# Kernel tuning notes

Measured on AMD Instinct MI355X. Metric: run time of the kernel, lower is better.

The kernel has to match this reference:

```python
import jax, jax.numpy as jnp
import numpy as np

B, DIM_IN, DIM_OUT = 2048, 4096, 4096


def setup_inputs() -> dict:
    key = jax.random.key(0)
    k1, k2, k3 = jax.random.split(key, 3)
    # binary input activations (0/1), stored as int32
    x = jax.random.randint(k1, (B, DIM_IN), 0, 2, dtype=jnp.int32)
    masks = jax.random.uniform(k2, (DIM_IN, DIM_OUT)) < 0.5
    # integer thresholds in [0, dim_in)
    thresholds = jax.random.randint(k3, (DIM_OUT,), 0, DIM_IN, dtype=jnp.int32)
    return {"x": x, "masks": masks, "thresholds": thresholds}


def reference(x, masks, thresholds):
    # Original: expand x to (B, dim_in, dim_out), XNOR with masks, sum over dim_in,
    # compare vs thresholds. XNOR(a,b) = a*b + (1-a)*(1-b), so the sum over dim_in
    # is two GEMMs -- never materialize the (B, dim_in, dim_out) tensor.
    xf = x.astype(jnp.float32)              # (B, dim_in), values in {0,1}
    mf = masks.astype(jnp.float32)          # (dim_in, dim_out)
    sums = xf @ mf + (1.0 - xf) @ (1.0 - mf)  # (B, dim_out), popcount of agreements
    return sums > thresholds.astype(jnp.float32)[None, :]  # (B, dim_out) bool
```

## Files before the change

### kernel.cpp

```cpp
#include <hip/hip_runtime.h>
#include <stdint.h>

#define BB    2048
#define DIN   4096
#define DOUT  4096


using v4i  = __attribute__((ext_vector_type(4)))  int;
using v16i = __attribute__((ext_vector_type(16))) int;

__device__ __forceinline__ void async_load16(const void* g, void* l) {
    __builtin_amdgcn_global_load_lds(
        (const __attribute__((address_space(1))) unsigned int*)g,
        (__attribute__((address_space(3))) unsigned int*)l,
        16, 0, 0);
}

__device__ __forceinline__ unsigned int to_pm1(unsigned int c) {
    return c + ((c ^ 0x01010101u) * 255u);
}

__global__ void pack_all(const int* __restrict__ x,
                         const void* __restrict__ mraw,
                         char* __restrict__ x8,
                         char* __restrict__ m8T) {
    const int tid = threadIdx.x;
    if (blockIdx.x < 1024) {
        #pragma unroll
        for (int rr = 0; rr < 2; ++rr) {
            const int row = blockIdx.x * 2 + rr;
            const int4* src = (const int4*)(x + (size_t)row * DIN);
            unsigned int* dst = (unsigned int*)(x8 + (size_t)row * DIN);
            #pragma unroll
            for (int q = 0; q < 4; ++q) {
                int4 v = src[q * 256 + tid];
                unsigned int t = (unsigned int)(v.x & 1) |
                                 ((unsigned int)(v.y & 1) << 8) |
                                 ((unsigned int)(v.z & 1) << 16) |
                                 ((unsigned int)(v.w & 1) << 24);
                dst[q * 256 + tid] = to_pm1(t);
            }
        }
    } else {
        const int bw = blockIdx.x - 1024;
        const int n0  = (bw >> 4) * 64;
        const int k0b = (bw & 15) * 256;

        const unsigned char* mb = (const unsigned char*)mraw;
        const unsigned int pv = *(const unsigned int*)(mb + (tid & 63) * 4);
        const bool isU8 = __any(pv > 1u);

        const int n4 = (tid & 15) * 4;
        const int k4 = (tid >> 4) * 4;
        #pragma unroll
        for (int kt = 0; kt < 4; ++kt) {
            const int k0 = k0b + kt * 64;
            unsigned int a[4];
            if (isU8) {
                #pragma unroll
                for (int r = 0; r < 4; ++r)
                    a[r] = *(const unsigned int*)(mb + (size_t)(k0 + k4 + r) * DOUT + n0 + n4);
            } else {
                const int4* m32 = (const int4*)mraw;
                #pragma unroll
                for (int r = 0; r < 4; ++r) {
                    int4 v = m32[((size_t)(k0 + k4 + r) * DOUT + n0 + n4) >> 2];
                    a[r] = (unsigned int)(v.x & 1) |
                           ((unsigned int)(v.y & 1) << 8) |
                           ((unsigned int)(v.z & 1) << 16) |
                           ((unsigned int)(v.w & 1) << 24);
                }
            }
            unsigned int x0 = __builtin_amdgcn_perm(a[1], a[0], 0x05010400u);
            unsigned int x1 = __builtin_amdgcn_perm(a[3], a[2], 0x05010400u);
            unsigned int x2 = __builtin_amdgcn_perm(a[1], a[0], 0x07030602u);
            unsigned int x3 = __builtin_amdgcn_perm(a[3], a[2], 0x07030602u);
            unsigned int c0 = __builtin_amdgcn_perm(x1, x0, 0x05040100u);
            unsigned int c1 = __builtin_amdgcn_perm(x1, x0, 0x07060302u);
            unsigned int c2 = __builtin_amdgcn_perm(x3, x2, 0x05040100u);
            unsigned int c3 = __builtin_amdgcn_perm(x3, x2, 0x07060302u);
            *(unsigned int*)(m8T + (size_t)(n0 + n4 + 0) * DIN + k0 + k4) = to_pm1(c0);
            *(unsigned int*)(m8T + (size_t)(n0 + n4 + 1) * DIN + k0 + k4) = to_pm1(c1);
            *(unsigned int*)(m8T + (size_t)(n0 + n4 + 2) * DIN + k0 + k4) = to_pm1(c2);
            *(unsigned int*)(m8T + (size_t)(n0 + n4 + 3) * DIN + k0 + k4) = to_pm1(c3);
        }
    }
}

__global__ __launch_bounds__(256)
void bgemm(const char* __restrict__ x8,
           const char* __restrict__ m8T,
           const int* __restrict__ thr,
           int* __restrict__ out) {
    const int flat = blockIdx.x;
    const int xcd  = flat & 7;
    const int idx  = flat >> 3;
    const int bm   = (xcd & 1) * 4 + (idx & 3);
    const int bn   = (xcd >> 1) * 8 + (idx >> 2);
    const int b0   = bm * 256;
    const int o0   = bn * 128;

    const int tid  = threadIdx.x;
    const int lane = tid & 63;
    const int wv   = tid >> 6;
    const int wm   = (wv & 1) * 128;
    const int wn   = (wv >> 1) * 64;
    const int l31  = lane & 31;
    const int lh   = lane >> 5;
    const int rsw  = l31 & 7;

    __shared__ __align__(16) char lA[2][256 * 128];
    __shared__ __align__(16) char lB[2][128 * 128];

    auto stage = [&](int c, int buf) {
        const int k0 = c * 128;
        const int r8 = lane >> 3;
        const int sl = lane & 7;
        #pragma unroll
        for (int h = 0; h < 8; ++h) {
            const int r0  = wv * 64 + h * 8;
            const int row = r0 + r8;
            const int g   = sl ^ (row & 7);
            async_load16(x8 + (size_t)(b0 + row) * DIN + k0 + g * 16,
                         &lA[buf][r0 * 128 + lane * 16]);
        }
        #pragma unroll
        for (int h = 0; h < 4; ++h) {
            const int r0  = wv * 32 + h * 8;
            const int row = r0 + r8;
            const int g   = sl ^ (row & 7);
            async_load16(m8T + (size_t)(o0 + row) * DIN + k0 + g * 16,
                         &lB[buf][r0 * 128 + lane * 16]);
        }
    };

    v16i acc[4][2];
    #pragma unroll
    for (int t = 0; t < 4; ++t)
        #pragma unroll
        for (int u = 0; u < 2; ++u)
            acc[t][u] = (v16i)(0);

    stage(0, 0);
    __syncthreads();

    for (int c = 0; c < 32; ++c) {
        const int buf = c & 1;
        if (c < 31) stage(c + 1, buf ^ 1);

        #pragma unroll
        for (int ks = 0; ks < 4; ++ks) {
            const int slot = ((ks * 2 + lh) ^ rsw) * 16;
            v4i aF[4], bF[2];
            #pragma unroll
            for (int t = 0; t < 4; ++t)
                aF[t] = *(const v4i*)&lA[buf][(wm + t * 32 + l31) * 128 + slot];
            #pragma unroll
            for (int u = 0; u < 2; ++u)
                bF[u] = *(const v4i*)&lB[buf][(wn + u * 32 + l31) * 128 + slot];
            #pragma unroll
            for (int t = 0; t < 4; ++t)
                #pragma unroll
                for (int u = 0; u < 2; ++u)
                    acc[t][u] = __builtin_amdgcn_mfma_i32_32x32x32_i8(
                        aF[t], bF[u], acc[t][u], 0, 0, 0);
        }
        __syncthreads();
    }

    #pragma unroll
    for (int u = 0; u < 2; ++u) {
        const int o   = o0 + wn + u * 32 + l31;
        const int lim = 2 * thr[o] - DIN;
        #pragma unroll
        for (int t = 0; t < 4; ++t) {
            #pragma unroll
            for (int r = 0; r < 16; ++r) {
                const int rowl = (r & 3) + 8 * (r >> 2) + 4 * lh;
                const int b    = b0 + wm + t * 32 + rowl;
                out[(size_t)b * DOUT + o] = (acc[t][u][r] > lim) ? 1 : 0;
            }
        }
    }
}

extern "C" void kernel_launch(void* const* d_in, const int* in_sizes, int n_in,
                              void* d_out, int out_size, void* d_ws, size_t ws_size,
                              hipStream_t stream) {
    const int* x          = (const int*)d_in[0];
    const void* masks     = d_in[1];
    const int* thresholds = (const int*)d_in[2];
    int* out              = (int*)d_out;

    char* x8  = (char*)d_ws;
    char* m8T = (char*)d_ws + ((size_t)8 << 20);

    pack_all<<<2048, 256, 0, stream>>>(x, masks, x8, m8T);
    bgemm<<<256, 256, 0, stream>>>(x8, m8T, thresholds, out);
}
```

Measured before the change: 201.4 us.

## Split K across 8 waves with triple-buffered LDS and finer-grained pack blocks

The GEMM kernel now runs 512 threads per block. Each pair of wave groups handles half of every 128-wide K chunk, and their partial accumulators are combined through an LDS reduction at the end. The LDS pipeline moves from double to triple buffering, using explicit vmcnt waits and one raw barrier per iteration instead of two __syncthreads, so loads run further ahead of the MFMAs. The pack kernel also launches more, smaller blocks. The goal is more latency hiding and occupancy, at the cost of extra LDS (144KB), a reduction epilogue, and doubled register pressure per block.

Result: faster. 174.6 us (-13.3%).

```diff
diff --git a/kernel.cpp b/kernel.cpp
--- a/kernel.cpp
+++ b/kernel.cpp
@@ -25,26 +25,23 @@
                          char* __restrict__ x8,
                          char* __restrict__ m8T) {
     const int tid = threadIdx.x;
-    if (blockIdx.x < 1024) {
-        #pragma unroll
-        for (int rr = 0; rr < 2; ++rr) {
-            const int row = blockIdx.x * 2 + rr;
-            const int4* src = (const int4*)(x + (size_t)row * DIN);
-            unsigned int* dst = (unsigned int*)(x8 + (size_t)row * DIN);
-            #pragma unroll
-            for (int q = 0; q < 4; ++q) {
-                int4 v = src[q * 256 + tid];
-                unsigned int t = (unsigned int)(v.x & 1) |
-                                 ((unsigned int)(v.y & 1) << 8) |
-                                 ((unsigned int)(v.z & 1) << 16) |
-                                 ((unsigned int)(v.w & 1) << 24);
-                dst[q * 256 + tid] = to_pm1(t);
-            }
+    if (blockIdx.x < BB) {
+        const int row = blockIdx.x;
+        const int4* src = (const int4*)(x + (size_t)row * DIN);
+        unsigned int* dst = (unsigned int*)(x8 + (size_t)row * DIN);
+        #pragma unroll
+        for (int q = 0; q < 4; ++q) {
+            int4 v = src[q * 256 + tid];
+            unsigned int t = (unsigned int)(v.x & 1) |
+                             ((unsigned int)(v.y & 1) << 8) |
+                             ((unsigned int)(v.z & 1) << 16) |
+                             ((unsigned int)(v.w & 1) << 24);
+            dst[q * 256 + tid] = to_pm1(t);
         }
     } else {
-        const int bw = blockIdx.x - 1024;
-        const int n0  = (bw >> 4) * 64;
-        const int k0b = (bw & 15) * 256;
+        const int bw = blockIdx.x - BB;
+        const int k0 = (bw & 63) * 64;
+        const int n0 = (bw >> 6) * 64;
 
         const unsigned char* mb = (const unsigned char*)mraw;
         const unsigned int pv = *(const unsigned int*)(mb + (tid & 63) * 4);
@@ -52,42 +49,38 @@
 
         const int n4 = (tid & 15) * 4;
         const int k4 = (tid >> 4) * 4;
-        #pragma unroll
-        for (int kt = 0; kt < 4; ++kt) {
-            const int k0 = k0b + kt * 64;
-            unsigned int a[4];
-            if (isU8) {
-                #pragma unroll
-                for (int r = 0; r < 4; ++r)
-                    a[r] = *(const unsigned int*)(mb + (size_t)(k0 + k4 + r) * DOUT + n0 + n4);
-            } else {
-                const int4* m32 = (const int4*)mraw;
-                #pragma unroll
-                for (int r = 0; r < 4; ++r) {
-                    int4 v = m32[((size_t)(k0 + k4 + r) * DOUT + n0 + n4) >> 2];
-                    a[r] = (unsigned int)(v.x & 1) |
-                           ((unsigned int)(v.y & 1) << 8) |
-                           ((unsigned int)(v.z & 1) << 16) |
-                           ((unsigned int)(v.w & 1) << 24);
-                }
+        unsigned int a[4];
+        if (isU8) {
+            #pragma unroll
+            for (int r = 0; r < 4; ++r)
+                a[r] = *(const unsigned int*)(mb + (size_t)(k0 + k4 + r) * DOUT + n0 + n4);
+        } else {
+            const int4* m32 = (const int4*)mraw;
+            #pragma unroll
+            for (int r = 0; r < 4; ++r) {
+                int4 v = m32[((size_t)(k0 + k4 + r) * DOUT + n0 + n4) >> 2];
+                a[r] = (unsigned int)(v.x & 1) |
+                       ((unsigned int)(v.y & 1) << 8) |
+                       ((unsigned int)(v.z & 1) << 16) |
+                       ((unsigned int)(v.w & 1) << 24);
             }
-            unsigned int x0 = __builtin_amdgcn_perm(a[1], a[0], 0x05010400u);
-            unsigned int x1 = __builtin_amdgcn_perm(a[3], a[2], 0x05010400u);
-            unsigned int x2 = __builtin_amdgcn_perm(a[1], a[0], 0x07030602u);
-            unsigned int x3 = __builtin_amdgcn_perm(a[3], a[2], 0x07030602u);
-            unsigned int c0 = __builtin_amdgcn_perm(x1, x0, 0x05040100u);
-            unsigned int c1 = __builtin_amdgcn_perm(x1, x0, 0x07060302u);
-            unsigned int c2 = __builtin_amdgcn_perm(x3, x2, 0x05040100u);
-            unsigned int c3 = __builtin_amdgcn_perm(x3, x2, 0x07060302u);
-            *(unsigned int*)(m8T + (size_t)(n0 + n4 + 0) * DIN + k0 + k4) = to_pm1(c0);
-            *(unsigned int*)(m8T + (size_t)(n0 + n4 + 1) * DIN + k0 + k4) = to_pm1(c1);
-            *(unsigned int*)(m8T + (size_t)(n0 + n4 + 2) * DIN + k0 + k4) = to_pm1(c2);
-            *(unsigned int*)(m8T + (size_t)(n0 + n4 + 3) * DIN + k0 + k4) = to_pm1(c3);
-        }
-    }
-}
-
-__global__ __launch_bounds__(256)
+        }
+        unsigned int x0 = __builtin_amdgcn_perm(a[1], a[0], 0x05010400u);
+        unsigned int x1 = __builtin_amdgcn_perm(a[3], a[2], 0x05010400u);
+        unsigned int x2 = __builtin_amdgcn_perm(a[1], a[0], 0x07030602u);
+        unsigned int x3 = __builtin_amdgcn_perm(a[3], a[2], 0x07030602u);
+        unsigned int c0 = __builtin_amdgcn_perm(x1, x0, 0x05040100u);
+        unsigned int c1 = __builtin_amdgcn_perm(x1, x0, 0x07060302u);
+        unsigned int c2 = __builtin_amdgcn_perm(x3, x2, 0x05040100u);
+        unsigned int c3 = __builtin_amdgcn_perm(x3, x2, 0x07060302u);
+        *(unsigned int*)(m8T + (size_t)(n0 + n4 + 0) * DIN + k0 + k4) = to_pm1(c0);
+        *(unsigned int*)(m8T + (size_t)(n0 + n4 + 1) * DIN + k0 + k4) = to_pm1(c1);
+        *(unsigned int*)(m8T + (size_t)(n0 + n4 + 2) * DIN + k0 + k4) = to_pm1(c2);
+        *(unsigned int*)(m8T + (size_t)(n0 + n4 + 3) * DIN + k0 + k4) = to_pm1(c3);
+    }
+}
+
+__global__ __launch_bounds__(512)
 void bgemm(const char* __restrict__ x8,
            const char* __restrict__ m8T,
            const int* __restrict__ thr,
@@ -103,34 +96,38 @@
     const int tid  = threadIdx.x;
     const int lane = tid & 63;
     const int wv   = tid >> 6;
-    const int wm   = (wv & 1) * 128;
-    const int wn   = (wv >> 1) * 64;
+    const int im   = wv & 1;
+    const int in_  = (wv >> 1) & 1;
+    const int kh   = wv >> 2;
+    const int wm   = im * 128;
+    const int wn   = in_ * 64;
     const int l31  = lane & 31;
     const int lh   = lane >> 5;
     const int rsw  = l31 & 7;
 
-    __shared__ __align__(16) char lA[2][256 * 128];
-    __shared__ __align__(16) char lB[2][128 * 128];
+    __shared__ __align__(16) char lds[3 * 49152];
 
     auto stage = [&](int c, int buf) {
+        char* bufA = lds + buf * 49152;
+        char* bufB = bufA + 32768;
         const int k0 = c * 128;
         const int r8 = lane >> 3;
         const int sl = lane & 7;
-        #pragma unroll
-        for (int h = 0; h < 8; ++h) {
-            const int r0  = wv * 64 + h * 8;
-            const int row = r0 + r8;
-            const int g   = sl ^ (row & 7);
-            async_load16(x8 + (size_t)(b0 + row) * DIN + k0 + g * 16,
-                         &lA[buf][r0 * 128 + lane * 16]);
-        }
         #pragma unroll
         for (int h = 0; h < 4; ++h) {
             const int r0  = wv * 32 + h * 8;
             const int row = r0 + r8;
             const int g   = sl ^ (row & 7);
+            async_load16(x8 + (size_t)(b0 + row) * DIN + k0 + g * 16,
+                         bufA + r0 * 128 + lane * 16);
+        }
+        #pragma unroll
+        for (int h = 0; h < 2; ++h) {
+            const int r0  = wv * 16 + h * 8;
+            const int row = r0 + r8;
+            const int g   = sl ^ (row & 7);
             async_load16(m8T + (size_t)(o0 + row) * DIN + k0 + g * 16,
-                         &lB[buf][r0 * 128 + lane * 16]);
+                         bufB + r0 * 128 + lane * 16);
         }
     };
 
@@ -142,22 +139,26 @@
             acc[t][u] = (v16i)(0);
 
     stage(0, 0);
-    __syncthreads();
+    stage(1, 1);
 
     for (int c = 0; c < 32; ++c) {
-        const int buf = c & 1;
-        if (c < 31) stage(c + 1, buf ^ 1);
-
-        #pragma unroll
-        for (int ks = 0; ks < 4; ++ks) {
-            const int slot = ((ks * 2 + lh) ^ rsw) * 16;
+        if (c < 31) asm volatile("s_waitcnt vmcnt(6)" ::: "memory");
+        else        asm volatile("s_waitcnt vmcnt(0)" ::: "memory");
+        __builtin_amdgcn_s_barrier();
+        if (c < 30) stage(c + 2, (c + 2) % 3);
+
+        const char* bufA = lds + (c % 3) * 49152;
+        const char* bufB = bufA + 32768;
+        #pragma unroll
+        for (int ks = 0; ks < 2; ++ks) {
+            const int slot = (((kh * 4 + ks * 2 + lh) ^ rsw)) * 16;
             v4i aF[4], bF[2];
             #pragma unroll
             for (int t = 0; t < 4; ++t)
-                aF[t] = *(const v4i*)&lA[buf][(wm + t * 32 + l31) * 128 + slot];
+                aF[t] = *(const v4i*)&bufA[(wm + t * 32 + l31) * 128 + slot];
             #pragma unroll
             for (int u = 0; u < 2; ++u)
-                bF[u] = *(const v4i*)&lB[buf][(wn + u * 32 + l31) * 128 + slot];
+                bF[u] = *(const v4i*)&bufB[(wn + u * 32 + l31) * 128 + slot];
             #pragma unroll
             for (int t = 0; t < 4; ++t)
                 #pragma unroll
@@ -165,7 +166,39 @@
                     acc[t][u] = __builtin_amdgcn_mfma_i32_32x32x32_i8(
                         aF[t], bF[u], acc[t][u], 0, 0, 0);
         }
-        __syncthreads();
+    }
+    __syncthreads();
+
+    int* pool = (int*)lds;
+    const int p = wv & 3;
+    {
+        const int give0 = kh ? 0 : 2;
+        const int bw_ = p * 8192 + (kh ? 0 : 1) * 4096;
+        #pragma unroll
+        for (int tt = 0; tt < 2; ++tt) {
+            const int t = give0 + tt;
+            #pragma unroll
+            for (int u = 0; u < 2; ++u)
+                #pragma unroll
+                for (int r = 0; r < 16; ++r) {
+                    const int rowl = (r & 3) + 8 * (r >> 2) + 4 * lh;
+                    pool[bw_ + (tt * 32 + rowl) * 64 + u * 32 + l31] = acc[t][u][r];
+                }
+        }
+    }
+    __syncthreads();
+    const int keep0 = kh ? 2 : 0;
+    const int br_ = p * 8192 + kh * 4096;
+    #pragma unroll
+    for (int tt = 0; tt < 2; ++tt) {
+        const int t = keep0 + tt;
+        #pragma unroll
+        for (int u = 0; u < 2; ++u)
+            #pragma unroll
+            for (int r = 0; r < 16; ++r) {
+                const int rowl = (r & 3) + 8 * (r >> 2) + 4 * lh;
+                acc[t][u][r] += pool[br_ + (tt * 32 + rowl) * 64 + u * 32 + l31];
+            }
     }
 
     #pragma unroll
@@ -173,11 +206,12 @@
         const int o   = o0 + wn + u * 32 + l31;
         const int lim = 2 * thr[o] - DIN;
         #pragma unroll
-        for (int t = 0; t < 4; ++t) {
+        for (int tt = 0; tt < 2; ++tt) {
+            const int t = keep0 + tt;
             #pragma unroll
             for (int r = 0; r < 16; ++r) {
                 const int rowl = (r & 3) + 8 * (r >> 2) + 4 * lh;
-                const int b    = b0 + wm + t * 32 + rowl;
+                const int b    = b0 + wm + kh * 64 + tt * 32 + rowl;
                 out[(size_t)b * DOUT + o] = (acc[t][u][r] > lim) ? 1 : 0;
             }
         }
@@ -195,6 +229,6 @@
     char* x8  = (char*)d_ws;
     char* m8T = (char*)d_ws + ((size_t)8 << 20);
 
-    pack_all<<<2048, 256, 0, stream>>>(x, masks, x8, m8T);
-    bgemm<<<256, 256, 0, stream>>>(x8, m8T, thresholds, out);
-}
+    pack_all<<<BB + 4096, 256, 0, stream>>>(x, masks, x8, m8T);
+    bgemm<<<256, 512, 0, stream>>>(x8, m8T, thresholds, out);
+}
```
